# Kernel tuning notes

Hardware: AMD Instinct MI355X
Metric: run time of the kernel (lower is better)

The kernel has to match this reference:

```python
import jax, jax.numpy as jnp
import numpy as np

LN_EPS = 1e-5

def _lstm_scan(xp, w_hh):
    # xp: [T, B, 4H] precomputed input projections (+bias); w_hh: [4H, H]
    H = w_hh.shape[1]
    B = xp.shape[1]
    def step(carry, x_t):
        h, c = carry
        gates = x_t + h @ w_hh.T
        i, f, g, o = jnp.split(gates, 4, axis=-1)  # torch gate order i,f,g,o
        i = jax.nn.sigmoid(i); f = jax.nn.sigmoid(f)
        g = jnp.tanh(g); o = jax.nn.sigmoid(o)
        c = f * c + i * g
        h = o * jnp.tanh(c)
        return (h, c), h
    init = (jnp.zeros((B, H), xp.dtype), jnp.zeros((B, H), xp.dtype))
    _, hs = jax.lax.scan(step, init, xp)
    return hs  # [T, B, H]

def setup_inputs() -> dict:
    key = jax.random.key(0)
    ks = jax.random.split(key, 16)
    B, T, V, E, K = 64, 512, 21128, 256, 9
    H4 = 4 * E
    s = 0.08  # small init scale for numerical stability
    return {
        'word_ids': jax.random.randint(ks[0], (B, T), 0, V, dtype=jnp.int32),
        'label_ids': jax.random.randint(ks[1], (B, T), 0, K, dtype=jnp.int32),
        'embed_table': jax.random.normal(ks[2], (V, E), jnp.float32) * s,
        'w_ih_f': jax.random.normal(ks[3], (H4, E), jnp.float32) * s,
        'w_hh_f': jax.random.normal(ks[4], (H4, E), jnp.float32) * s,
        'b_f': jnp.zeros((H4,), jnp.float32),
        'w_ih_b': jax.random.normal(ks[5], (H4, E), jnp.float32) * s,
        'w_hh_b': jax.random.normal(ks[6], (H4, E), jnp.float32) * s,
        'b_b': jnp.zeros((H4,), jnp.float32),
        'ln_gamma': jnp.ones((2 * E,), jnp.float32),
        'ln_beta': jnp.zeros((2 * E,), jnp.float32),
        'cls_w': jax.random.normal(ks[7], (K, 2 * E), jnp.float32) * s,
        'cls_b': jnp.zeros((K,), jnp.float32),
        'crf_start': jax.random.normal(ks[8], (K,), jnp.float32) * 0.1,
        'crf_end': jax.random.normal(ks[9], (K,), jnp.float32) * 0.1,
        'crf_trans': jax.random.normal(ks[10], (K, K), jnp.float32) * 0.1,
    }

def reference(word_ids, label_ids, embed_table, w_ih_f, w_hh_f, b_f,
              w_ih_b, w_hh_b, b_b, ln_gamma, ln_beta, cls_w, cls_b,
              crf_start, crf_end, crf_trans):
    # Embedding (dropout is identity at eval)
    emb = embed_table[word_ids]                      # [B, T, E]

    # BiLSTM: precompute input projections once, scan over time
    xf = (emb @ w_ih_f.T + b_f).transpose(1, 0, 2)   # [T, B, 4H]
    hf = _lstm_scan(xf, w_hh_f)                      # [T, B, H]
    xb = (emb[:, ::-1] @ w_ih_b.T + b_b).transpose(1, 0, 2)
    hb = _lstm_scan(xb, w_hh_b)[::-1]                # reverse back to forward time
    seq = jnp.concatenate([hf, hb], axis=-1).transpose(1, 0, 2)  # [B, T, 2H]

    # LayerNorm over last dim
    mu = seq.mean(-1, keepdims=True)
    var = ((seq - mu) ** 2).mean(-1, keepdims=True)
    seq = (seq - mu) * jax.lax.rsqrt(var + LN_EPS) * ln_gamma + ln_beta

    logits = seq @ cls_w.T + cls_b                   # [B, T, K] = CRF emissions

    # --- CRF log-likelihood (no mask: all positions valid) ---
    tags = label_ids
    # numerator: score of gold path
    em_score = jnp.take_along_axis(logits, tags[..., None], axis=-1)[..., 0]  # [B, T]
    trans_score = crf_trans[tags[:, :-1], tags[:, 1:]].sum(axis=1)            # [B]
    numerator = (crf_start[tags[:, 0]] + em_score.sum(axis=1)
                 + trans_score + crf_end[tags[:, -1]])                        # [B]

    # denominator: forward algorithm (logsumexp DP over time)
    alpha0 = crf_start[None, :] + logits[:, 0]       # [B, K]
    em_rest = logits[:, 1:].transpose(1, 0, 2)       # [T-1, B, K]
    def step(alpha, em_t):
        # alpha: [B, K] (prev tag), crf_trans: [K, K], em_t: [B, K] (next tag)
        new = jax.scipy.special.logsumexp(
            alpha[:, :, None] + crf_trans[None, :, :] + em_t[:, None, :], axis=1)
        return new, None
    alpha, _ = jax.lax.scan(step, alpha0, em_rest)
    logZ = jax.scipy.special.logsumexp(alpha + crf_end[None, :], axis=1)      # [B]

    llh = (numerator - logZ).sum()   # torchcrf default reduction='sum'
    loss = -llh
    preds = jnp.argmax(logits, axis=-1)
    return (loss, preds)
```

## Files before the change

### kernel.cpp

```cpp
#include <hip/hip_runtime.h>
#include <cstdint>
#include <cmath>

typedef __attribute__((ext_vector_type(8))) short short8;
typedef __attribute__((ext_vector_type(4))) float floatx4;

__device__ __forceinline__ unsigned pk_bf16(float x, float y) {
    unsigned ux = __float_as_uint(x); ux = ux + 0x7fffu + ((ux >> 16) & 1u);
    unsigned uy = __float_as_uint(y); uy = uy + 0x7fffu + ((uy >> 16) & 1u);
    return (ux >> 16) | (uy & 0xffff0000u);
}
__device__ __forceinline__ unsigned short bf16r(float x) {
    unsigned ux = __float_as_uint(x);
    return (unsigned short)((ux + 0x7fffu + ((ux >> 16) & 1u)) >> 16);
}
__device__ __forceinline__ float bf16d(unsigned short v) {
    return __uint_as_float((unsigned)v << 16);
}

__global__ __launch_bounds__(256) void proj_kernel(
    const int* __restrict__ word_ids, const float* __restrict__ embed,
    const float* __restrict__ w_ih_f, const float* __restrict__ b_f,
    const float* __restrict__ w_ih_b, const float* __restrict__ b_b,
    unsigned short* __restrict__ XF, unsigned short* __restrict__ XB,
    int t0, int lgL)
{
    __shared__ unsigned short As[64][264];
    __shared__ unsigned short Bs[64][264];
    __shared__ int idx[64];

    const int tid = threadIdx.x;
    const int jt  = blockIdx.x;
    const int nt  = blockIdx.y;
    const int dir = blockIdx.z;
    const int Lm1 = (1 << lgL) - 1;
    const float* __restrict__ W    = dir ? w_ih_b : w_ih_f;
    const float* __restrict__ bias = dir ? b_b : b_f;
    unsigned short* __restrict__ Xout = dir ? XB : XF;

    if (tid < 64) {
        int n  = nt * 64 + tid;
        int b  = n >> lgL;
        int tl = n & Lm1;
        int tg = dir ? (511 - (t0 + tl)) : (t0 + tl);
        idx[tid] = word_ids[b * 512 + tg];
    }
    __syncthreads();

    #pragma unroll
    for (int i = 0; i < 16; ++i) {
        int flat = i * 256 + tid;
        int r  = flat >> 6;
        int kq = flat & 63;
        floatx4 a = *(const floatx4*)&embed[(size_t)idx[r] * 256 + kq * 4];
        *(uint2*)&As[r][kq * 4] = make_uint2(pk_bf16(a.x, a.y), pk_bf16(a.z, a.w));
        floatx4 wv = *(const floatx4*)&W[(size_t)(jt * 64 + r) * 256 + kq * 4];
        *(uint2*)&Bs[r][kq * 4] = make_uint2(pk_bf16(wv.x, wv.y), pk_bf16(wv.z, wv.w));
    }
    __syncthreads();

    const int w    = tid >> 6;
    const int lane = tid & 63;
    const int q    = lane >> 4;
    const int lr   = lane & 15;

    short8 af[8];
    #pragma unroll
    for (int ks = 0; ks < 8; ++ks)
        af[ks] = *(const short8*)&As[w * 16 + lr][ks * 32 + q * 8];

    floatx4 acc[4];
    #pragma unroll
    for (int jt4 = 0; jt4 < 4; ++jt4) {
        floatx4 c = {0.f, 0.f, 0.f, 0.f};
        #pragma unroll
        for (int ks = 0; ks < 8; ++ks) {
            short8 bf = *(const short8*)&Bs[jt4 * 16 + lr][ks * 32 + q * 8];
            c = __builtin_amdgcn_mfma_f32_16x16x32_bf16(af[ks], bf, c, 0, 0, 0);
        }
        acc[jt4] = c;
    }

    #pragma unroll
    for (int jt4 = 0; jt4 < 4; ++jt4) {
        int j = jt * 64 + jt4 * 16 + lr;
        float bj = bias[j];
        #pragma unroll
        for (int reg = 0; reg < 4; ++reg) {
            int n  = nt * 64 + w * 16 + q * 4 + reg;
            int b  = n >> lgL;
            int tl = n & Lm1;
            Xout[((size_t)tl * 64 + b) * 1024 + j] = bf16r(acc[jt4][reg] + bj);
        }
    }
}

__global__ __launch_bounds__(512, 1)
__attribute__((amdgpu_num_vgpr(256)))
void lstm_scan(
    const unsigned short* __restrict__ XF, const unsigned short* __restrict__ XB,
    const float* __restrict__ w_hh_f, const float* __restrict__ w_hh_b,
    float* __restrict__ hf, float* __restrict__ hb,
    float* __restrict__ state_c, float* __restrict__ state_h, int t0, int t1)
{
    __shared__ unsigned short Ah[2][264];
    __shared__ float scr[4][2][256];
    __shared__ short8 Wlds[8 * 2 * 8 * 64];

    const int blk = blockIdx.x;
    const int dir = blk >> 5;
    const int grp = blk & 31;
    const int B0  = grp * 2;
    const unsigned short* __restrict__ X = dir ? XB : XF;
    const float* __restrict__ Whh = dir ? w_hh_b : w_hh_f;
    float* __restrict__ Hout      = dir ? hb : hf;

    const int tid  = threadIdx.x;
    const int w    = tid >> 6;
    const int lane = tid & 63;
    const int q    = lane >> 4;
    const int lr   = lane & 15;
    const int g    = w >> 1;
    const int uh   = w & 1;

    short8 wreg[6][8];
    #pragma unroll
    for (int ntl = 0; ntl < 8; ++ntl) {
        const float* wrow = &Whh[(size_t)(g * 256 + uh * 128 + ntl * 16 + lr) * 256];
        #pragma unroll
        for (int ks = 0; ks < 8; ++ks) {
            floatx4 a = *(const floatx4*)&wrow[ks * 32 + q * 8];
            floatx4 b = *(const floatx4*)&wrow[ks * 32 + q * 8 + 4];
            union { uint4 u4; short8 s; } cv;
            cv.u4 = make_uint4(pk_bf16(a.x, a.y), pk_bf16(a.z, a.w),
                               pk_bf16(b.x, b.y), pk_bf16(b.z, b.w));
            if (ntl < 6) wreg[ntl][ks] = cv.s;
            else         Wlds[((w * 2 + (ntl - 6)) * 8 + ks) * 64 + lane] = cv.s;
        }
    }

    const int b_p = tid >> 8;
    const int u_p = tid & 255;
    const int sgi = (dir * 64 + B0 + b_p) * 256 + u_p;
    float cst = 0.f;
    float hlast = 0.f;
    if (t0 == 0) {
        Ah[b_p][u_p] = 0;
    } else {
        cst = state_c[sgi];
        hlast = state_h[sgi];
        Ah[b_p][u_p] = bf16r(hlast);
    }

    for (int t = t0; t < t1; ++t) {
        float xg[4];
        {
            const unsigned short* Xc = &X[((size_t)(t - t0) * 64 + B0 + b_p) * 1024 + u_p];
            #pragma unroll
            for (int gg = 0; gg < 4; ++gg)
                xg[gg] = bf16d(Xc[gg * 256]);
        }
        __syncthreads();

        short8 af[8];
        #pragma unroll
        for (int ks = 0; ks < 8; ++ks)
            af[ks] = *(const short8*)&Ah[lr & 1][ks * 32 + q * 8];
        #pragma unroll
        for (int ntl = 0; ntl < 8; ++ntl) {
            floatx4 c = {0.f, 0.f, 0.f, 0.f};
            #pragma unroll
            for (int ks = 0; ks < 8; ++ks) {
                if (ntl < 6)
                    c = __builtin_amdgcn_mfma_f32_16x16x32_bf16(af[ks], wreg[ntl][ks], c, 0, 0, 0);
                else
                    c = __builtin_amdgcn_mfma_f32_16x16x32_bf16(
                            af[ks], Wlds[((w * 2 + (ntl - 6)) * 8 + ks) * 64 + lane], c, 0, 0, 0);
            }
            if (q == 0) {
                scr[g][0][uh * 128 + ntl * 16 + lr] = c[0];
                scr[g][1][uh * 128 + ntl * 16 + lr] = c[1];
            }
        }
        __syncthreads();

        {
            float gi = scr[0][b_p][u_p] + xg[0];
            float gf = scr[1][b_p][u_p] + xg[1];
            float gg = scr[2][b_p][u_p] + xg[2];
            float go = scr[3][b_p][u_p] + xg[3];
            float ig = 1.f / (1.f + expf(-gi));
            float fg = 1.f / (1.f + expf(-gf));
            float gv = tanhf(gg);
            float og = 1.f / (1.f + expf(-go));
            cst = fg * cst + ig * gv;
            float h = og * tanhf(cst);
            hlast = h;
            int tt = dir ? (511 - t) : t;
            Hout[((size_t)tt * 64 + B0 + b_p) * 256 + u_p] = h;
            Ah[b_p][u_p] = bf16r(h);
        }
    }

    state_c[sgi] = cst;
    state_h[sgi] = hlast;
}

__global__ __launch_bounds__(256) void ln_cls_kernel(
    const float* __restrict__ hf, const float* __restrict__ hb,
    const float* __restrict__ gamma, const float* __restrict__ beta,
    const float* __restrict__ cls_w, const float* __restrict__ cls_b,
    float* __restrict__ logits, float* __restrict__ dout)
{
    const int lane = threadIdx.x & 63;
    const int wid  = threadIdx.x >> 6;
    const int pos  = blockIdx.x * 4 + wid;
    const int b = pos >> 9;
    const int t = pos & 511;

    float4 v0 = *(const float4*)&hf[((size_t)t * 64 + b) * 256 + lane * 4];
    float4 v1 = *(const float4*)&hb[((size_t)t * 64 + b) * 256 + lane * 4];
    float x[8] = {v0.x, v0.y, v0.z, v0.w, v1.x, v1.y, v1.z, v1.w};

    float s = 0.f;
    #pragma unroll
    for (int i = 0; i < 8; ++i) s += x[i];
    #pragma unroll
    for (int off = 32; off > 0; off >>= 1) s += __shfl_xor(s, off, 64);
    float mu = s * (1.f / 512.f);

    float d[8];
    float sq = 0.f;
    #pragma unroll
    for (int i = 0; i < 8; ++i) { d[i] = x[i] - mu; sq += d[i] * d[i]; }
    #pragma unroll
    for (int off = 32; off > 0; off >>= 1) sq += __shfl_xor(sq, off, 64);
    float rs = 1.f / sqrtf(sq * (1.f / 512.f) + 1e-5f);

    float4 g0  = *(const float4*)&gamma[lane * 4];
    float4 g1  = *(const float4*)&gamma[256 + lane * 4];
    float4 be0 = *(const float4*)&beta[lane * 4];
    float4 be1 = *(const float4*)&beta[256 + lane * 4];
    float y[8];
    y[0] = d[0] * rs * g0.x + be0.x; y[1] = d[1] * rs * g0.y + be0.y;
    y[2] = d[2] * rs * g0.z + be0.z; y[3] = d[3] * rs * g0.w + be0.w;
    y[4] = d[4] * rs * g1.x + be1.x; y[5] = d[5] * rs * g1.y + be1.y;
    y[6] = d[6] * rs * g1.z + be1.z; y[7] = d[7] * rs * g1.w + be1.w;

    float lgt[9];
    #pragma unroll
    for (int c = 0; c < 9; ++c) {
        float4 w0 = *(const float4*)&cls_w[c * 512 + lane * 4];
        float4 w1 = *(const float4*)&cls_w[c * 512 + 256 + lane * 4];
        float p = y[0] * w0.x + y[1] * w0.y + y[2] * w0.z + y[3] * w0.w
                + y[4] * w1.x + y[5] * w1.y + y[6] * w1.z + y[7] * w1.w;
        #pragma unroll
        for (int off = 32; off > 0; off >>= 1) p += __shfl_xor(p, off, 64);
        lgt[c] = p + cls_b[c];
    }
    if (lane == 0) {
        int bestc = 0;
        float bestv = lgt[0];
        #pragma unroll
        for (int c = 1; c < 9; ++c)
            if (lgt[c] > bestv) { bestv = lgt[c]; bestc = c; }
        dout[1 + pos] = (float)bestc;
        #pragma unroll
        for (int c = 0; c < 9; ++c) logits[(size_t)pos * 9 + c] = lgt[c];
    }
}

__global__ __launch_bounds__(64) void crf_kernel(
    const float* __restrict__ logits, const int* __restrict__ label_ids,
    const float* __restrict__ crf_start, const float* __restrict__ crf_end,
    const float* __restrict__ crf_trans, float* __restrict__ llh)
{
    __shared__ float Ts[9][12];
    const int b = blockIdx.x;
    const int lane = threadIdx.x;
    if (lane < 81) Ts[lane / 9][lane % 9] = crf_trans[lane];
    __syncthreads();

    const float* __restrict__ em  = &logits[(size_t)b * 512 * 9];
    const int* __restrict__ tags  = &label_ids[b * 512];

    float part = 0.f;
    for (int t = lane; t < 512; t += 64) {
        int tg = tags[t];
        part += em[t * 9 + tg];
        if (t < 511) part += Ts[tg][tags[t + 1]];
    }
    #pragma unroll
    for (int off = 32; off > 0; off >>= 1) part += __shfl_xor(part, off, 64);
    float numer = part + crf_start[tags[0]] + crf_end[tags[511]];

    const int j = (lane < 9) ? lane : 0;
    float alpha = crf_start[j] + em[j];
    for (int t = 1; t < 512; ++t) {
        float av[9];
        float m = -1e30f;
        #pragma unroll
        for (int i = 0; i < 9; ++i) {
            float ai = __shfl(alpha, i, 64);
            av[i] = ai + Ts[i][j];
            m = fmaxf(m, av[i]);
        }
        float ssum = 0.f;
        #pragma unroll
        for (int i = 0; i < 9; ++i) ssum += expf(av[i] - m);
        alpha = m + logf(ssum) + em[t * 9 + j];
    }
    float v = (lane < 9) ? (alpha + crf_end[j]) : -1e30f;
    float mm = v;
    #pragma unroll
    for (int off = 32; off > 0; off >>= 1) mm = fmaxf(mm, __shfl_xor(mm, off, 64));
    float es = (lane < 9) ? expf(v - mm) : 0.f;
    #pragma unroll
    for (int off = 32; off > 0; off >>= 1) es += __shfl_xor(es, off, 64);
    if (lane == 0) llh[b] = numer - (mm + logf(es));
}

__global__ __launch_bounds__(64) void final_reduce(
    const float* __restrict__ llh, float* __restrict__ dout)
{
    float v = llh[threadIdx.x];
    #pragma unroll
    for (int off = 32; off > 0; off >>= 1) v += __shfl_xor(v, off, 64);
    if (threadIdx.x == 0) dout[0] = -v;
}

extern "C" void kernel_launch(void* const* d_in, const int* in_sizes, int n_in,
                              void* d_out, int out_size, void* d_ws, size_t ws_size,
                              hipStream_t stream)
{
    const int*   word_ids  = (const int*)d_in[0];
    const int*   label_ids = (const int*)d_in[1];
    const float* embed     = (const float*)d_in[2];
    const float* w_ih_f    = (const float*)d_in[3];
    const float* w_hh_f    = (const float*)d_in[4];
    const float* b_f       = (const float*)d_in[5];
    const float* w_ih_b    = (const float*)d_in[6];
    const float* w_hh_b    = (const float*)d_in[7];
    const float* b_b       = (const float*)d_in[8];
    const float* ln_gamma  = (const float*)d_in[9];
    const float* ln_beta   = (const float*)d_in[10];
    const float* cls_w     = (const float*)d_in[11];
    const float* cls_b     = (const float*)d_in[12];
    const float* crf_start = (const float*)d_in[13];
    const float* crf_end   = (const float*)d_in[14];
    const float* crf_trans = (const float*)d_in[15];

    char* w = (char*)d_ws;
    auto alloc = [&](size_t bytes) -> char* {
        char* p = w; w += (bytes + 255) & ~(size_t)255; return p;
    };
    float* hf      = (float*)alloc((size_t)8388608 * 4);
    float* hb      = (float*)alloc((size_t)8388608 * 4);
    float* logits  = (float*)alloc((size_t)294912 * 4);
    float* state_c = (float*)alloc((size_t)32768 * 4);
    float* state_h = (float*)alloc((size_t)32768 * 4);
    float* llh     = (float*)alloc((size_t)64 * 4);
    size_t fixed   = (size_t)(w - (char*)d_ws);

    int L = 512;
    while (L > 32 && fixed + (size_t)L * 262144 > ws_size) L >>= 1;
    unsigned short* XF = (unsigned short*)alloc((size_t)L * 65536 * 2);
    unsigned short* XB = (unsigned short*)alloc((size_t)L * 65536 * 2);
    int lgL = 31 - __builtin_clz((unsigned)L);

    for (int t0 = 0; t0 < 512; t0 += L) {
        proj_kernel<<<dim3(16, L, 2), 256, 0, stream>>>(
            word_ids, embed, w_ih_f, b_f, w_ih_b, b_b, XF, XB, t0, lgL);
        lstm_scan<<<64, 512, 0, stream>>>(
            XF, XB, w_hh_f, w_hh_b, hf, hb, state_c, state_h, t0, t0 + L);
    }
    ln_cls_kernel<<<8192, 256, 0, stream>>>(
        hf, hb, ln_gamma, ln_beta, cls_w, cls_b, logits, (float*)d_out);
    crf_kernel<<<64, 64, 0, stream>>>(
        logits, label_ids, crf_start, crf_end, crf_trans, llh);
    final_reduce<<<1, 64, 0, stream>>>(llh, (float*)d_out);
}
```

Before: 1.539 ms.

## Split LSTM recurrence matmul across 16 waves with 1024-thread blocks

Doubles the LSTM scan block size from 512 to 1024 threads, so each of 16 waves computes 4 output tiles of the recurrent matmul instead of 8. This halves the serial MFMA chain per wave on every time step. The four accumulator chains are now interleaved within the k-loop for more instruction-level parallelism. Weights go 3 tiles to registers and 1 to LDS per wave, and the gate math stays on the first 512 threads, which leaves half the threads idle during that phase and adds barrier cost for more waves.

```diff
diff --git a/kernel.cpp b/kernel.cpp
--- a/kernel.cpp
+++ b/kernel.cpp
@@ -95,9 +95,7 @@
     }
 }
 
-__global__ __launch_bounds__(512, 1)
-__attribute__((amdgpu_num_vgpr(256)))
-void lstm_scan(
+__global__ __launch_bounds__(1024, 1) void lstm_scan(
     const unsigned short* __restrict__ XF, const unsigned short* __restrict__ XB,
     const float* __restrict__ w_hh_f, const float* __restrict__ w_hh_b,
     float* __restrict__ hf, float* __restrict__ hb,
@@ -105,7 +103,7 @@
 {
     __shared__ unsigned short Ah[2][264];
     __shared__ float scr[4][2][256];
-    __shared__ short8 Wlds[8 * 2 * 8 * 64];
+    __shared__ short8 Wlds[16 * 8 * 64];
 
     const int blk = blockIdx.x;
     const int dir = blk >> 5;
@@ -120,13 +118,13 @@
     const int lane = tid & 63;
     const int q    = lane >> 4;
     const int lr   = lane & 15;
-    const int g    = w >> 1;
-    const int uh   = w & 1;
-
-    short8 wreg[6][8];
-    #pragma unroll
-    for (int ntl = 0; ntl < 8; ++ntl) {
-        const float* wrow = &Whh[(size_t)(g * 256 + uh * 128 + ntl * 16 + lr) * 256];
+    const int g    = w >> 2;
+    const int qt   = w & 3;
+
+    short8 wreg[3][8];
+    #pragma unroll
+    for (int ntl = 0; ntl < 4; ++ntl) {
+        const float* wrow = &Whh[(size_t)(g * 256 + qt * 64 + ntl * 16 + lr) * 256];
         #pragma unroll
         for (int ks = 0; ks < 8; ++ks) {
             floatx4 a = *(const floatx4*)&wrow[ks * 32 + q * 8];
@@ -134,8 +132,8 @@
             union { uint4 u4; short8 s; } cv;
             cv.u4 = make_uint4(pk_bf16(a.x, a.y), pk_bf16(a.z, a.w),
                                pk_bf16(b.x, b.y), pk_bf16(b.z, b.w));
-            if (ntl < 6) wreg[ntl][ks] = cv.s;
-            else         Wlds[((w * 2 + (ntl - 6)) * 8 + ks) * 64 + lane] = cv.s;
+            if (ntl < 3) wreg[ntl][ks] = cv.s;
+            else         Wlds[(w * 8 + ks) * 64 + lane] = cv.s;
         }
     }
 
@@ -145,8 +143,8 @@
     float cst = 0.f;
     float hlast = 0.f;
     if (t0 == 0) {
-        Ah[b_p][u_p] = 0;
-    } else {
+        for (int i = tid; i < 528; i += 1024) ((unsigned short*)Ah)[i] = 0;
+    } else if (tid < 512) {
         cst = state_c[sgi];
         hlast = state_h[sgi];
         Ah[b_p][u_p] = bf16r(hlast);
@@ -154,7 +152,7 @@
 
     for (int t = t0; t < t1; ++t) {
         float xg[4];
-        {
+        if (tid < 512) {
             const unsigned short* Xc = &X[((size_t)(t - t0) * 64 + B0 + b_p) * 1024 + u_p];
             #pragma unroll
             for (int gg = 0; gg < 4; ++gg)
@@ -162,29 +160,26 @@
         }
         __syncthreads();
 
-        short8 af[8];
-        #pragma unroll
-        for (int ks = 0; ks < 8; ++ks)
-            af[ks] = *(const short8*)&Ah[lr & 1][ks * 32 + q * 8];
-        #pragma unroll
-        for (int ntl = 0; ntl < 8; ++ntl) {
-            floatx4 c = {0.f, 0.f, 0.f, 0.f};
-            #pragma unroll
-            for (int ks = 0; ks < 8; ++ks) {
-                if (ntl < 6)
-                    c = __builtin_amdgcn_mfma_f32_16x16x32_bf16(af[ks], wreg[ntl][ks], c, 0, 0, 0);
-                else
-                    c = __builtin_amdgcn_mfma_f32_16x16x32_bf16(
-                            af[ks], Wlds[((w * 2 + (ntl - 6)) * 8 + ks) * 64 + lane], c, 0, 0, 0);
-            }
-            if (q == 0) {
-                scr[g][0][uh * 128 + ntl * 16 + lr] = c[0];
-                scr[g][1][uh * 128 + ntl * 16 + lr] = c[1];
-            }
+        floatx4 c0 = {0,0,0,0}, c1 = {0,0,0,0}, c2 = {0,0,0,0}, c3 = {0,0,0,0};
+        #pragma unroll
+        for (int ks = 0; ks < 8; ++ks) {
+            short8 a = *(const short8*)&Ah[lr & 1][ks * 32 + q * 8];
+            short8 w3 = Wlds[(w * 8 + ks) * 64 + lane];
+            c0 = __builtin_amdgcn_mfma_f32_16x16x32_bf16(a, wreg[0][ks], c0, 0, 0, 0);
+            c1 = __builtin_amdgcn_mfma_f32_16x16x32_bf16(a, wreg[1][ks], c1, 0, 0, 0);
+            c2 = __builtin_amdgcn_mfma_f32_16x16x32_bf16(a, wreg[2][ks], c2, 0, 0, 0);
+            c3 = __builtin_amdgcn_mfma_f32_16x16x32_bf16(a, w3, c3, 0, 0, 0);
+        }
+        if (q == 0) {
+            int ub = qt * 64 + lr;
+            scr[g][0][ub]      = c0[0];  scr[g][1][ub]      = c0[1];
+            scr[g][0][ub + 16] = c1[0];  scr[g][1][ub + 16] = c1[1];
+            scr[g][0][ub + 32] = c2[0];  scr[g][1][ub + 32] = c2[1];
+            scr[g][0][ub + 48] = c3[0];  scr[g][1][ub + 48] = c3[1];
         }
         __syncthreads();
 
-        {
+        if (tid < 512) {
             float gi = scr[0][b_p][u_p] + xg[0];
             float gf = scr[1][b_p][u_p] + xg[1];
             float gg = scr[2][b_p][u_p] + xg[2];
@@ -202,8 +197,10 @@
         }
     }
 
-    state_c[sgi] = cst;
-    state_h[sgi] = hlast;
+    if (tid < 512) {
+        state_c[sgi] = cst;
+        state_h[sgi] = hlast;
+    }
 }
 
 __global__ __launch_bounds__(256) void ln_cls_kernel(
@@ -371,7 +368,7 @@
     for (int t0 = 0; t0 < 512; t0 += L) {
         proj_kernel<<<dim3(16, L, 2), 256, 0, stream>>>(
             word_ids, embed, w_ih_f, b_f, w_ih_b, b_b, XF, XB, t0, lgL);
-        lstm_scan<<<64, 512, 0, stream>>>(
+        lstm_scan<<<64, 1024, 0, stream>>>(
             XF, XB, w_hh_f, w_hh_b, hf, hb, state_c, state_h, t0, t0 + L);
     }
     ln_cls_kernel<<<8192, 256, 0, stream>>>(
```

Result: slower. 2.089 ms (+35.7%).
